# Performance work log

Hardware: AMD Instinct MI355X
Metric: run time of the kernel (lower is better)

The kernel has to match this reference:

```python
import jax, jax.numpy as jnp
import numpy as np
import math

B, T, C, H = 4, 1024, 1024, 16
D = C // H
EPS = 1e-5

def layer_norm(x, gamma, beta):
    mu = jnp.mean(x, axis=-1, keepdims=True)
    var = jnp.var(x, axis=-1, keepdims=True)
    return (x - mu) * jax.lax.rsqrt(var + EPS) * gamma + beta

def setup_inputs() -> dict:
    key = jax.random.key(0)
    ks = jax.random.split(key, 12)
    s = 0.02
    return {
        "x": jax.random.normal(ks[0], (B, T, C), dtype=jnp.float32),
        "attn_mask": jax.random.randint(ks[1], (B, 1, 1, T), 0, 2, dtype=jnp.int32),
        "Wq": jax.random.normal(ks[2], (C, C), dtype=jnp.float32) * s,
        "bq": jnp.zeros((C,), dtype=jnp.float32),
        "Wk": jax.random.normal(ks[3], (C, C), dtype=jnp.float32) * s,
        "bk": jnp.zeros((C,), dtype=jnp.float32),
        "Wv": jax.random.normal(ks[4], (C, C), dtype=jnp.float32) * s,
        "bv": jnp.zeros((C,), dtype=jnp.float32),
        "Wo": jax.random.normal(ks[5], (C, C), dtype=jnp.float32) * s,
        "bo": jnp.zeros((C,), dtype=jnp.float32),
        "ln_g": jnp.ones((C,), dtype=jnp.float32),
        "ln_b": jnp.zeros((C,), dtype=jnp.float32),
    }

def reference(x, attn_mask, Wq, bq, Wk, bk, Wv, bv, Wo, bo, ln_g, ln_b):
    # projections -> [B, H, T, D]
    def split_heads(y):
        return y.reshape(B, T, H, D).transpose(0, 2, 1, 3)
    q = split_heads(x @ Wq + bq)
    k = split_heads(x @ Wk + bk)
    v = split_heads(x @ Wv + bv)
    scale = 1.0 / math.sqrt(D)
    wei = jnp.einsum('bhqd,bhkd->bhqk', q, k) * scale  # [B,H,T,T]
    wei = jnp.where(attn_mask == 0, jnp.float32(-jnp.inf), wei)
    wei = jax.nn.softmax(wei, axis=-1)
    out = jnp.einsum('bhqk,bhkd->bhqd', wei, v)
    out = out.transpose(0, 2, 1, 3).reshape(B, T, C)
    out = out @ Wo + bo
    return layer_norm(out, ln_g, ln_b)
```

## Files before the change

### kernel.cpp

```cpp
#include <hip/hip_runtime.h>
#include <stdint.h>

#define B_ 4
#define T_ 1024
#define C_ 1024
#define H_ 16
#define D_ 64
#define M_ 4096

typedef __attribute__((ext_vector_type(8))) short bf16x8;
typedef __attribute__((ext_vector_type(4))) float f32x4;
typedef __attribute__((ext_vector_type(4))) short short4v;

static __device__ __forceinline__ short f2bf(float f) {
  union { float f; unsigned u; } c; c.f = f;
  unsigned r = (c.u + 0x7fffu + ((c.u >> 16) & 1u)) >> 16;
  return (short)(unsigned short)r;
}

static __device__ __forceinline__ void gl2lds16(const void* g, void* l) {
  __builtin_amdgcn_global_load_lds(
      (const __attribute__((address_space(1))) void*)(uintptr_t)g,
      (__attribute__((address_space(3))) void*)(uint32_t)(uintptr_t)l,
      16, 0, 0);
}

__global__ __launch_bounds__(256) void k_cast_x(const float* __restrict__ x,
                                                short* __restrict__ xb) {
  int i = blockIdx.x * 256 + threadIdx.x;
  float4 v = ((const float4*)x)[i];
  short4v o;
  o.x = f2bf(v.x); o.y = f2bf(v.y); o.z = f2bf(v.z); o.w = f2bf(v.w);
  ((short4v*)xb)[i] = o;
}

__global__ void k_transpose_w(const float* __restrict__ Wq, const float* __restrict__ Wk,
                              const float* __restrict__ Wv, const float* __restrict__ Wo,
                              short* __restrict__ Wt) {
  __shared__ float t[32][33];
  const float* W = (blockIdx.z == 0) ? Wq : (blockIdx.z == 1) ? Wk
                   : (blockIdx.z == 2) ? Wv : Wo;
  short* out = Wt + (size_t)blockIdx.z * C_ * C_;
  int n0 = blockIdx.x * 32, k0 = blockIdx.y * 32;
  int tx = threadIdx.x, ty = threadIdx.y;
#pragma unroll
  for (int i = 0; i < 4; i++)
    t[ty + 8*i][tx] = W[(size_t)(k0 + ty + 8*i) * C_ + n0 + tx];
  __syncthreads();
#pragma unroll
  for (int i = 0; i < 4; i++)
    out[(size_t)(n0 + ty + 8*i) * C_ + k0 + tx] = f2bf(t[tx][ty + 8*i]);
}

static __device__ __forceinline__ void gemm_body(const short* __restrict__ A,
                                                 const short* __restrict__ Bt,
                                                 short* sA, short* sB,
                                                 f32x4 acc[4][4]) {
  const int tid = threadIdx.x;
  const int w = tid >> 6, lane = tid & 63;
  const int quad = lane >> 4, l16 = lane & 15;
  const int m0 = blockIdx.y * 128, n0 = blockIdx.x * 128;
  const int wm = (w >> 1) * 64, wn = (w & 1) * 64;
  const int srow = lane >> 3;
  const int sch = lane & 7;

#pragma unroll
  for (int mt = 0; mt < 4; mt++)
#pragma unroll
    for (int nt = 0; nt < 4; nt++)
#pragma unroll
      for (int e = 0; e < 4; e++) acc[mt][nt][e] = 0.f;

  for (int k0 = 0; k0 < C_; k0 += 64) {
    __syncthreads();
#pragma unroll
    for (int i = 0; i < 4; i++) {
      int c = w * 4 + i;
      int row = c * 8 + srow;
      int ch = sch ^ (row & 7);
      gl2lds16(&A[(size_t)(m0 + row) * C_ + k0 + ch * 8], &sA[c * 512]);
      gl2lds16(&Bt[(size_t)(n0 + row) * C_ + k0 + ch * 8], &sB[c * 512]);
    }
    __syncthreads();
#pragma unroll
    for (int ks = 0; ks < 2; ks++) {
      bf16x8 af[4], bfv[4];
      int chq = ks * 4 + quad;
#pragma unroll
      for (int t4 = 0; t4 < 4; t4++) {
        int rowa = wm + t4 * 16 + l16;
        af[t4] = *(const bf16x8*)&sA[rowa * 64 + (chq ^ (rowa & 7)) * 8];
        int rowb = wn + t4 * 16 + l16;
        bfv[t4] = *(const bf16x8*)&sB[rowb * 64 + (chq ^ (rowb & 7)) * 8];
      }
#pragma unroll
      for (int mt = 0; mt < 4; mt++)
#pragma unroll
        for (int nt = 0; nt < 4; nt++)
          acc[mt][nt] = __builtin_amdgcn_mfma_f32_16x16x32_bf16(
              af[mt], bfv[nt], acc[mt][nt], 0, 0, 0);
    }
  }
}

__global__ __launch_bounds__(256) void k_qkv(
    const short* __restrict__ A, const short* __restrict__ WtAll,
    const float* __restrict__ bq, const float* __restrict__ bk,
    const float* __restrict__ bv,
    short* __restrict__ Qb, short* __restrict__ Kb, short* __restrict__ Vtb) {
  __shared__ short sU[17408];
  const int mode = blockIdx.z;
  const short* Bt = WtAll + (size_t)mode * C_ * C_;
  const float* bias = (mode == 0) ? bq : (mode == 1) ? bk : bv;
  f32x4 acc[4][4];
  gemm_body(A, Bt, sU, sU + 8192, acc);

  const int tid = threadIdx.x;
  const int w = tid >> 6, lane = tid & 63;
  const int quad = lane >> 4, l16 = lane & 15;
  const int m0 = blockIdx.y * 128, n0 = blockIdx.x * 128;
  const int wm = (w >> 1) * 64, wn = (w & 1) * 64;

  if (mode < 2) {
#pragma unroll
    for (int mt = 0; mt < 4; mt++) {
#pragma unroll
      for (int nt = 0; nt < 4; nt++) {
        int ng = n0 + wn + nt * 16 + l16;
        float bval = bias[ng];
        int h = ng >> 6, d = ng & 63;
#pragma unroll
        for (int r = 0; r < 4; r++) {
          int mg = m0 + wm + mt * 16 + quad * 4 + r;
          int bb = mg >> 10, t = mg & 1023;
          short v16 = f2bf(acc[mt][nt][r] + bval);
          if (mode == 0)
            Qb[(((size_t)(bb * H_ + h) << 10) + t) * D_ + d] = v16;
          else
            Kb[(((size_t)(bb * H_ + h) << 10) + t) * D_ + d] = v16;
        }
      }
    }
  } else {
    __syncthreads();
#pragma unroll
    for (int nt = 0; nt < 4; nt++) {
      int nl = wn + nt * 16 + l16;
      float bval = bias[n0 + nl];
#pragma unroll
      for (int mt = 0; mt < 4; mt++)
#pragma unroll
        for (int r = 0; r < 4; r++)
          sU[nl * 136 + wm + mt * 16 + quad * 4 + r] = f2bf(acc[mt][nt][r] + bval);
    }
    __syncthreads();
    int dr = tid >> 1;
    int dg = n0 + dr, hd = dg >> 6, dl = dg & 63;
    int bb2 = m0 >> 10, t0 = m0 & 1023;
    size_t base = (((size_t)(bb2 * H_ + hd) * D_ + dl) << 10) + t0;
#pragma unroll
    for (int i = 0; i < 8; i++) {
      int jj = (tid & 1) * 8 + i;
      *(int4*)&Vtb[base + jj * 8] = *(const int4*)&sU[dr * 136 + jj * 8];
    }
  }
}

__global__ __launch_bounds__(256) void k_proj(
    const short* __restrict__ A, const short* __restrict__ Bt,
    const float* __restrict__ bias, float* __restrict__ Y) {
  __shared__ short sA[8192];
  __shared__ short sB[8192];
  f32x4 acc[4][4];
  gemm_body(A, Bt, sA, sB, acc);

  const int tid = threadIdx.x;
  const int w = tid >> 6, lane = tid & 63;
  const int quad = lane >> 4, l16 = lane & 15;
  const int m0 = blockIdx.y * 128, n0 = blockIdx.x * 128;
  const int wm = (w >> 1) * 64, wn = (w & 1) * 64;

#pragma unroll
  for (int mt = 0; mt < 4; mt++)
#pragma unroll
    for (int nt = 0; nt < 4; nt++) {
      int ng = n0 + wn + nt * 16 + l16;
      float bval = bias[ng];
#pragma unroll
      for (int r = 0; r < 4; r++) {
        int mg = m0 + wm + mt * 16 + quad * 4 + r;
        Y[(size_t)mg * C_ + ng] = acc[mt][nt][r] + bval;
      }
    }
}

#define PSTRIDE 136
__global__ __launch_bounds__(256, 2) void k_attn(
    const short* __restrict__ Qb, const short* __restrict__ Kb,
    const short* __restrict__ Vtb, const int* __restrict__ mask,
    short* __restrict__ Ob) {
  __shared__ short sK[8192];
  __shared__ short sV[8192];
  __shared__ short sP[4 * 32 * PSTRIDE];
  __shared__ float sBias[1024];
  const int tid = threadIdx.x;
  const int w = tid >> 6, lane = tid & 63;
  const int quad = lane >> 4, l16 = lane & 15;

  const int bx = blockIdx.x;
  const int xcd = bx & 7, j = bx >> 3;
  const int qb = j & 7, u = j >> 3;
  const int h = xcd * 2 + (u & 1), bb = u >> 1;
  const int tq0 = qb * 128 + w * 32;

  const short* Qh = Qb + ((size_t)(bb * H_ + h) << 10) * D_;
  const short* Kh = Kb + ((size_t)(bb * H_ + h) << 10) * D_;
  const short* Vh = Vtb + (((size_t)(bb * H_ + h) * D_) << 10);
  const int* mrow = mask + bb * T_;
  short* Pw = &sP[w * 32 * PSTRIDE];

  const float SC = 0.125f * 1.44269504088896340736f;

  {
    int4 m4 = ((const int4*)mrow)[tid];
    float4 bv4;
    bv4.x = m4.x ? 0.f : -1e30f; bv4.y = m4.y ? 0.f : -1e30f;
    bv4.z = m4.z ? 0.f : -1e30f; bv4.w = m4.w ? 0.f : -1e30f;
    ((float4*)sBias)[tid] = bv4;
  }

  bf16x8 aq[2][2];
#pragma unroll
  for (int rt = 0; rt < 2; rt++)
#pragma unroll
    for (int ks = 0; ks < 2; ks++)
      aq[rt][ks] = *(const bf16x8*)&Qh[(size_t)(tq0 + rt * 16 + l16) * D_ +
                                       ks * 32 + quad * 8];

  f32x4 o[2][4];
  float lsum[2][4];
#pragma unroll
  for (int rt = 0; rt < 2; rt++) {
#pragma unroll
    for (int nt = 0; nt < 4; nt++)
#pragma unroll
      for (int e = 0; e < 4; e++) o[rt][nt][e] = 0.f;
#pragma unroll
    for (int r = 0; r < 4; r++) lsum[rt][r] = 0.f;
  }

  for (int kt = 0; kt < T_; kt += 128) {
    __syncthreads();
#pragma unroll
    for (int i2 = 0; i2 < 4; i2++) {
      int i = w * 4 + i2;
      int row = i * 8 + (lane >> 3);
      int g = (lane & 7) ^ (row & 7);
      gl2lds16(&Kh[(size_t)(kt + row) * D_ + g * 8], &sK[i * 512]);
    }
#pragma unroll
    for (int i2 = 0; i2 < 4; i2++) {
      int i = w * 4 + i2;
      int row = i * 4 + (lane >> 4);
      int g = (lane & 15) ^ (row & 15);
      gl2lds16(&Vh[((size_t)row << 10) + kt + g * 8], &sV[i * 512]);
    }
    __syncthreads();

    f32x4 s[2][8];
#pragma unroll
    for (int rt = 0; rt < 2; rt++)
#pragma unroll
      for (int ct = 0; ct < 8; ct++)
#pragma unroll
        for (int e = 0; e < 4; e++) s[rt][ct][e] = 0.f;

#pragma unroll
    for (int ks = 0; ks < 2; ks++)
#pragma unroll
      for (int ct = 0; ct < 8; ct++) {
        int rowb = ct * 16 + l16;
        bf16x8 bk8 = *(const bf16x8*)&sK[rowb * 64 +
                                         (((ks * 4 + quad) ^ (rowb & 7)) * 8)];
        s[0][ct] = __builtin_amdgcn_mfma_f32_16x16x32_bf16(aq[0][ks], bk8, s[0][ct], 0, 0, 0);
        s[1][ct] = __builtin_amdgcn_mfma_f32_16x16x32_bf16(aq[1][ks], bk8, s[1][ct], 0, 0, 0);
      }

    float mb[8];
#pragma unroll
    for (int ct = 0; ct < 8; ct++) mb[ct] = sBias[kt + ct * 16 + l16];

#pragma unroll
    for (int rt = 0; rt < 2; rt++)
#pragma unroll
      for (int ct = 0; ct < 8; ct++)
#pragma unroll
        for (int r = 0; r < 4; r++) {
          float p = __builtin_amdgcn_exp2f(fmaf(s[rt][ct][r], SC, mb[ct]));
          lsum[rt][r] += p;
          Pw[(rt * 16 + quad * 4 + r) * PSTRIDE + ct * 16 + l16] = f2bf(p);
        }

#pragma unroll
    for (int ks2 = 0; ks2 < 4; ks2++) {
      bf16x8 pa0 = *(const bf16x8*)&Pw[l16 * PSTRIDE + ks2 * 32 + quad * 8];
      bf16x8 pa1 = *(const bf16x8*)&Pw[(16 + l16) * PSTRIDE + ks2 * 32 + quad * 8];
#pragma unroll
      for (int nt = 0; nt < 4; nt++) {
        int rowv = nt * 16 + l16;
        bf16x8 bv8 = *(const bf16x8*)&sV[rowv * 128 +
                                         (((ks2 * 4 + quad) ^ (rowv & 15)) * 8)];
        o[0][nt] = __builtin_amdgcn_mfma_f32_16x16x32_bf16(pa0, bv8, o[0][nt], 0, 0, 0);
        o[1][nt] = __builtin_amdgcn_mfma_f32_16x16x32_bf16(pa1, bv8, o[1][nt], 0, 0, 0);
      }
    }
  }

#pragma unroll
  for (int rt = 0; rt < 2; rt++)
#pragma unroll
    for (int r = 0; r < 4; r++) {
      float rs = lsum[rt][r];
#pragma unroll
      for (int off = 1; off < 16; off <<= 1) rs += __shfl_xor(rs, off);
      float inv = 1.f / rs;
      int tg = tq0 + rt * 16 + quad * 4 + r;
#pragma unroll
      for (int nt = 0; nt < 4; nt++) {
        int col = h * D_ + nt * 16 + l16;
        Ob[(size_t)(bb * T_ + tg) * C_ + col] = f2bf(o[rt][nt][r] * inv);
      }
    }
}

__global__ __launch_bounds__(256) void k_ln(float* __restrict__ Y,
                                            const float* __restrict__ g,
                                            const float* __restrict__ b) {
  __shared__ float red[4], red2[4];
  const int row = blockIdx.x, tid = threadIdx.x;
  float4* yp = (float4*)(Y + (size_t)row * C_);
  float4 v = yp[tid];
  float sm = v.x + v.y + v.z + v.w;
#pragma unroll
  for (int off = 32; off; off >>= 1) sm += __shfl_xor(sm, off);
  if ((tid & 63) == 0) red[tid >> 6] = sm;
  __syncthreads();
  float mu = (red[0] + red[1] + red[2] + red[3]) * (1.f / C_);
  float dx = v.x - mu, dy = v.y - mu, dz = v.z - mu, dw = v.w - mu;
  float q = dx * dx + dy * dy + dz * dz + dw * dw;
#pragma unroll
  for (int off = 32; off; off >>= 1) q += __shfl_xor(q, off);
  if ((tid & 63) == 0) red2[tid >> 6] = q;
  __syncthreads();
  float var = (red2[0] + red2[1] + red2[2] + red2[3]) * (1.f / C_);
  float rsq = rsqrtf(var + 1e-5f);
  float4 gg = ((const float4*)g)[tid];
  float4 bb = ((const float4*)b)[tid];
  float4 out;
  out.x = dx * rsq * gg.x + bb.x;
  out.y = dy * rsq * gg.y + bb.y;
  out.z = dz * rsq * gg.z + bb.z;
  out.w = dw * rsq * gg.w + bb.w;
  yp[tid] = out;
}

extern "C" void kernel_launch(void* const* d_in, const int* in_sizes, int n_in,
                              void* d_out, int out_size, void* d_ws, size_t ws_size,
                              hipStream_t stream) {
  (void)in_sizes; (void)n_in; (void)out_size; (void)ws_size;
  const float* x    = (const float*)d_in[0];
  const int*   mask = (const int*)d_in[1];
  const float* Wq   = (const float*)d_in[2];
  const float* bq   = (const float*)d_in[3];
  const float* Wk   = (const float*)d_in[4];
  const float* bk   = (const float*)d_in[5];
  const float* Wv   = (const float*)d_in[6];
  const float* bv   = (const float*)d_in[7];
  const float* Wo   = (const float*)d_in[8];
  const float* bo   = (const float*)d_in[9];
  const float* lng  = (const float*)d_in[10];
  const float* lnb  = (const float*)d_in[11];

  char* ws = (char*)d_ws;
  short* xb  = (short*)(ws);
  short* Wt  = (short*)(ws + ((size_t)8  << 20));
  short* Qb  = (short*)(ws + ((size_t)16 << 20));
  short* Kb  = (short*)(ws + ((size_t)24 << 20));
  short* Vtb = (short*)(ws + ((size_t)32 << 20));
  short* Ob  = xb;
  float* Y   = (float*)d_out;

  k_cast_x<<<dim3(4096), dim3(256), 0, stream>>>(x, xb);
  k_transpose_w<<<dim3(32, 32, 4), dim3(32, 8), 0, stream>>>(Wq, Wk, Wv, Wo, Wt);
  k_qkv<<<dim3(8, 32, 3), dim3(256), 0, stream>>>(xb, Wt, bq, bk, bv, Qb, Kb, Vtb);
  k_attn<<<dim3(512), dim3(256), 0, stream>>>(Qb, Kb, Vtb, mask, Ob);
  k_proj<<<dim3(8, 32), dim3(256), 0, stream>>>(Ob, Wt + (size_t)3 * C_ * C_, bo, Y);
  k_ln<<<dim3(4096), dim3(256), 0, stream>>>(Y, lng, lnb);
}
```

Before: 209.3 us.

## Merge prep kernels, interleave QKV block order, halve proj M-tile

Merges the x cast and the weight transpose into one k_prep launch, which saves a kernel launch. The QKV GEMM grid is flattened so that blocks for Q, K and V sharing the same A tile sit next to each other, which should improve L2 reuse of the activation tile. The output projection uses 64x128 tiles instead of 128x128, doubling its block count to 512 so more of the GPU's CUs have work. In exchange, the smaller tiles give less data reuse per block and add a branchy load split across warps.

```diff
diff --git a/kernel.cpp b/kernel.cpp
--- a/kernel.cpp
+++ b/kernel.cpp
@@ -25,24 +25,28 @@
       16, 0, 0);
 }
 
-__global__ __launch_bounds__(256) void k_cast_x(const float* __restrict__ x,
-                                                short* __restrict__ xb) {
-  int i = blockIdx.x * 256 + threadIdx.x;
-  float4 v = ((const float4*)x)[i];
-  short4v o;
-  o.x = f2bf(v.x); o.y = f2bf(v.y); o.z = f2bf(v.z); o.w = f2bf(v.w);
-  ((short4v*)xb)[i] = o;
-}
-
-__global__ void k_transpose_w(const float* __restrict__ Wq, const float* __restrict__ Wk,
-                              const float* __restrict__ Wv, const float* __restrict__ Wo,
-                              short* __restrict__ Wt) {
+__global__ __launch_bounds__(256) void k_prep(
+    const float* __restrict__ x, short* __restrict__ xb,
+    const float* __restrict__ Wq, const float* __restrict__ Wk,
+    const float* __restrict__ Wv, const float* __restrict__ Wo,
+    short* __restrict__ Wt) {
   __shared__ float t[32][33];
-  const float* W = (blockIdx.z == 0) ? Wq : (blockIdx.z == 1) ? Wk
-                   : (blockIdx.z == 2) ? Wv : Wo;
-  short* out = Wt + (size_t)blockIdx.z * C_ * C_;
-  int n0 = blockIdx.x * 32, k0 = blockIdx.y * 32;
-  int tx = threadIdx.x, ty = threadIdx.y;
+  const int id = blockIdx.x, tid = threadIdx.x;
+  if (id < 4096) {
+    int i = id * 256 + tid;
+    float4 v = ((const float4*)x)[i];
+    short4v o;
+    o.x = f2bf(v.x); o.y = f2bf(v.y); o.z = f2bf(v.z); o.w = f2bf(v.w);
+    ((short4v*)xb)[i] = o;
+    return;
+  }
+  int j = id - 4096;
+  int bz = j >> 10, r = j & 1023;
+  int by = r >> 5, bx = r & 31;
+  const float* W = (bz == 0) ? Wq : (bz == 1) ? Wk : (bz == 2) ? Wv : Wo;
+  short* out = Wt + (size_t)bz * C_ * C_;
+  int n0 = bx * 32, k0 = by * 32;
+  int tx = tid & 31, ty = tid >> 5;
 #pragma unroll
   for (int i = 0; i < 4; i++)
     t[ty + 8*i][tx] = W[(size_t)(k0 + ty + 8*i) * C_ + n0 + tx];
@@ -55,11 +59,10 @@
 static __device__ __forceinline__ void gemm_body(const short* __restrict__ A,
                                                  const short* __restrict__ Bt,
                                                  short* sA, short* sB,
-                                                 f32x4 acc[4][4]) {
+                                                 f32x4 acc[4][4], int m0, int n0) {
   const int tid = threadIdx.x;
   const int w = tid >> 6, lane = tid & 63;
   const int quad = lane >> 4, l16 = lane & 15;
-  const int m0 = blockIdx.y * 128, n0 = blockIdx.x * 128;
   const int wm = (w >> 1) * 64, wn = (w & 1) * 64;
   const int srow = lane >> 3;
   const int sch = lane & 7;
@@ -109,16 +112,19 @@
     const float* __restrict__ bv,
     short* __restrict__ Qb, short* __restrict__ Kb, short* __restrict__ Vtb) {
   __shared__ short sU[17408];
-  const int mode = blockIdx.z;
+  const int id = blockIdx.x;
+  const int mode = id % 3;
+  const int j = id / 3;
+  const int bx = j & 7, by = j >> 3;
+  const int m0 = by * 128, n0 = bx * 128;
   const short* Bt = WtAll + (size_t)mode * C_ * C_;
   const float* bias = (mode == 0) ? bq : (mode == 1) ? bk : bv;
   f32x4 acc[4][4];
-  gemm_body(A, Bt, sU, sU + 8192, acc);
+  gemm_body(A, Bt, sU, sU + 8192, acc, m0, n0);
 
   const int tid = threadIdx.x;
   const int w = tid >> 6, lane = tid & 63;
   const int quad = lane >> 4, l16 = lane & 15;
-  const int m0 = blockIdx.y * 128, n0 = blockIdx.x * 128;
   const int wm = (w >> 1) * 64, wn = (w & 1) * 64;
 
   if (mode < 2) {
@@ -169,19 +175,65 @@
 __global__ __launch_bounds__(256) void k_proj(
     const short* __restrict__ A, const short* __restrict__ Bt,
     const float* __restrict__ bias, float* __restrict__ Y) {
-  __shared__ short sA[8192];
+  __shared__ short sA[4096];
   __shared__ short sB[8192];
-  f32x4 acc[4][4];
-  gemm_body(A, Bt, sA, sB, acc);
-
   const int tid = threadIdx.x;
   const int w = tid >> 6, lane = tid & 63;
   const int quad = lane >> 4, l16 = lane & 15;
-  const int m0 = blockIdx.y * 128, n0 = blockIdx.x * 128;
-  const int wm = (w >> 1) * 64, wn = (w & 1) * 64;
-
-#pragma unroll
-  for (int mt = 0; mt < 4; mt++)
+  const int m0 = blockIdx.y * 64, n0 = blockIdx.x * 128;
+  const int wm = (w >> 1) * 32, wn = (w & 1) * 64;
+  const int srow = lane >> 3, sch = lane & 7;
+
+  f32x4 acc[2][4];
+#pragma unroll
+  for (int mt = 0; mt < 2; mt++)
+#pragma unroll
+    for (int nt = 0; nt < 4; nt++)
+#pragma unroll
+      for (int e = 0; e < 4; e++) acc[mt][nt][e] = 0.f;
+
+  for (int k0 = 0; k0 < C_; k0 += 64) {
+    __syncthreads();
+#pragma unroll
+    for (int i = 0; i < 6; i++) {
+      int c = w * 6 + i;
+      if (c < 8) {
+        int row = c * 8 + srow;
+        int ch = sch ^ (row & 7);
+        gl2lds16(&A[(size_t)(m0 + row) * C_ + k0 + ch * 8], &sA[c * 512]);
+      } else {
+        int c2 = c - 8;
+        int row = c2 * 8 + srow;
+        int ch = sch ^ (row & 7);
+        gl2lds16(&Bt[(size_t)(n0 + row) * C_ + k0 + ch * 8], &sB[c2 * 512]);
+      }
+    }
+    __syncthreads();
+#pragma unroll
+    for (int ks = 0; ks < 2; ks++) {
+      bf16x8 af[2], bfv[4];
+      int chq = ks * 4 + quad;
+#pragma unroll
+      for (int t2 = 0; t2 < 2; t2++) {
+        int rowa = wm + t2 * 16 + l16;
+        af[t2] = *(const bf16x8*)&sA[rowa * 64 + (chq ^ (rowa & 7)) * 8];
+      }
+#pragma unroll
+      for (int t4 = 0; t4 < 4; t4++) {
+        int rowb = wn + t4 * 16 + l16;
+        bfv[t4] = *(const bf16x8*)&sB[rowb * 64 + (chq ^ (rowb & 7)) * 8];
+      }
+#pragma unroll
+      for (int mt = 0; mt < 2; mt++)
+#pragma unroll
+        for (int nt = 0; nt < 4; nt++)
+          acc[mt][nt] = __builtin_amdgcn_mfma_f32_16x16x32_bf16(
+              af[mt], bfv[nt], acc[mt][nt], 0, 0, 0);
+    }
+  }
+
+#pragma unroll
+  for (int mt = 0; mt < 2; mt++)
 #pragma unroll
     for (int nt = 0; nt < 4; nt++) {
       int ng = n0 + wn + nt * 16 + l16;
@@ -390,10 +442,9 @@
   short* Ob  = xb;
   float* Y   = (float*)d_out;
 
-  k_cast_x<<<dim3(4096), dim3(256), 0, stream>>>(x, xb);
-  k_transpose_w<<<dim3(32, 32, 4), dim3(32, 8), 0, stream>>>(Wq, Wk, Wv, Wo, Wt);
-  k_qkv<<<dim3(8, 32, 3), dim3(256), 0, stream>>>(xb, Wt, bq, bk, bv, Qb, Kb, Vtb);
+  k_prep<<<dim3(8192), dim3(256), 0, stream>>>(x, xb, Wq, Wk, Wv, Wo, Wt);
+  k_qkv<<<dim3(768), dim3(256), 0, stream>>>(xb, Wt, bq, bk, bv, Qb, Kb, Vtb);
   k_attn<<<dim3(512), dim3(256), 0, stream>>>(Qb, Kb, Vtb, mask, Ob);
-  k_proj<<<dim3(8, 32), dim3(256), 0, stream>>>(Ob, Wt + (size_t)3 * C_ * C_, bo, Y);
+  k_proj<<<dim3(8, 64), dim3(256), 0, stream>>>(Ob, Wt + (size_t)3 * C_ * C_, bo, Y);
   k_ln<<<dim3(4096), dim3(256), 0, stream>>>(Y, lng, lnb);
 }
```

New measurement: 199.5 us. 1.05x faster.
